# Performance work log

Measured on AMD Instinct MI355X. Metric: run time of the kernel, lower is better.

Reference implementation:

```python
import jax, jax.numpy as jnp
import numpy as np

K = 9            # base neighbors
MAX_DILATION = 3


def setup_inputs() -> dict:
    key = jax.random.key(0)
    x = jax.random.normal(key, (64, 256, 1024), dtype=jnp.float32)  # (B, C, N)
    return {"x": x, "layer_idx": 8}


def reference(x, layer_idx):
    # x: (B, C, N); layer_idx: python int
    B, C, N = x.shape
    dilation = min(layer_idx // 4 + 1, MAX_DILATION)
    k_d = K * dilation

    pts = jnp.transpose(x, (0, 2, 1))  # (B, N, C) points per graph segment
    # squared euclidean pairwise distances (same neighbor ordering as euclidean)
    sq = jnp.sum(pts * pts, axis=-1)                       # (B, N)
    d2 = sq[:, :, None] + sq[:, None, :] \
         - 2.0 * jnp.einsum('bnc,bmc->bnm', pts, pts)      # (B, N, N)

    # k_d nearest neighbors of each node (self included, as in DGL bruteforce knn)
    _, idx = jax.lax.top_k(-d2, k_d)                       # (B, N, k_d)

    # segmented graph: offset node ids per batch element
    offs = (jnp.arange(B) * N)[:, None, None]
    src = (idx + offs).reshape(-1)                         # neighbor -> node edges
    dst = jnp.repeat(jnp.arange(B * N), k_d)

    # dilation: take every `dilation`-th edge; since k_d = K*dilation and each
    # node's edges are contiguous, every node keeps exactly K edges
    src_d = src[::dilation]
    dst_d = dst[::dilation]
    # eval mode: no stochastic edge dropout; include_self=False -> no added self loops
    return src_d, dst_d
```

## Files before the change

kernel.cpp:

```cpp
#include <hip/hip_runtime.h>


typedef __bf16 bf16x8 __attribute__((ext_vector_type(8)));
typedef float  f32x4  __attribute__((ext_vector_type(4)));
typedef unsigned int u32;

#define B_   64
#define C_   256
#define N_   1024
#define NSRC (B_ * N_ * 9)

#define STRIDE_I 1088
#define REGION_W 8704

__device__ __forceinline__ u32 umin_(u32 a, u32 b) { return a < b ? a : b; }
__device__ __forceinline__ u32 umax_(u32 a, u32 b) { return a > b ? a : b; }

__device__ __forceinline__ void load_lds16(const void* g, void* l) {
    __builtin_amdgcn_global_load_lds((const __attribute__((address_space(1))) void*)g,
                                     (__attribute__((address_space(3))) void*)l,
                                     16, 0, 0);
}

__global__ __launch_bounds__(256, 4) void trans_kernel(const float* __restrict__ X,
                                                       unsigned short* __restrict__ XT,
                                                       float* __restrict__ NRM) {
    __shared__ u32 T2[128][66];
    const int tid = threadIdx.x;
    const int b   = blockIdx.x >> 4;
    const int n0  = (blockIdx.x & 15) * 64;

    {
        const int cpl = tid >> 4;
        const int s   = tid & 15;
#pragma unroll
        for (int it = 0; it < 8; ++it) {
            const int c0 = it * 32 + cpl * 2;
            const float* src = X + ((size_t)b * C_ + c0) * N_ + n0 + s * 4;
            float4 f0 = *(const float4*)(src);
            float4 f1 = *(const float4*)(src + N_);
            const float a0[4] = {f0.x, f0.y, f0.z, f0.w};
            const float a1[4] = {f1.x, f1.y, f1.z, f1.w};
            u32 pk[4];
#pragma unroll
            for (int j = 0; j < 4; ++j) {
                u32 u0 = __float_as_uint(a0[j]);
                u32 u1 = __float_as_uint(a1[j]);
                u32 b0 = (u0 + 0x7FFFu + ((u0 >> 16) & 1u)) >> 16;
                u32 b1 = (u1 + 0x7FFFu + ((u1 >> 16) & 1u)) >> 16;
                pk[j] = b0 | (b1 << 16);
            }
            *(uint4*)&T2[it * 16 + cpl][s * 4] = make_uint4(pk[0], pk[1], pk[2], pk[3]);
        }
    }
    __syncthreads();

    {
        const int rr = tid >> 2, p = tid & 3;
        unsigned short* xtrow = XT + ((size_t)b * N_ + n0 + rr) * C_;
        float nsq = 0.f;
#pragma unroll
        for (int j = 0; j < 8; ++j) {
            u32 x0 = T2[j * 16 + 4 * p + 0][rr];
            u32 x1 = T2[j * 16 + 4 * p + 1][rr];
            u32 x2 = T2[j * 16 + 4 * p + 2][rr];
            u32 x3 = T2[j * 16 + 4 * p + 3][rr];
            const u32 xs[4] = {x0, x1, x2, x3};
#pragma unroll
            for (int q = 0; q < 4; ++q) {
                float lo = __uint_as_float(xs[q] << 16);
                float hi = __uint_as_float(xs[q] & 0xFFFF0000u);
                nsq = fmaf(lo, lo, fmaf(hi, hi, nsq));
            }
            *(uint4*)((char*)xtrow + j * 64 + p * 16) = make_uint4(x0, x1, x2, x3);
        }
        nsq += __shfl_xor(nsq, 1);
        nsq += __shfl_xor(nsq, 2);
        if (p == 0) NRM[b * N_ + n0 + rr] = nsq;
    }
}

#define SORT8(v)                                                              \
    do {                                                                      \
        u32 mn, mx;                                                           \
        mn = umin_(v[0], v[4]); mx = umax_(v[0], v[4]); v[0] = mn; v[4] = mx; \
        mn = umin_(v[1], v[5]); mx = umax_(v[1], v[5]); v[1] = mn; v[5] = mx; \
        mn = umin_(v[2], v[6]); mx = umax_(v[2], v[6]); v[2] = mn; v[6] = mx; \
        mn = umin_(v[3], v[7]); mx = umax_(v[3], v[7]); v[3] = mn; v[7] = mx; \
        mn = umin_(v[0], v[2]); mx = umax_(v[0], v[2]); v[0] = mn; v[2] = mx; \
        mn = umin_(v[1], v[3]); mx = umax_(v[1], v[3]); v[1] = mn; v[3] = mx; \
        mn = umin_(v[4], v[6]); mx = umax_(v[4], v[6]); v[4] = mn; v[6] = mx; \
        mn = umin_(v[5], v[7]); mx = umax_(v[5], v[7]); v[5] = mn; v[7] = mx; \
        mn = umin_(v[0], v[1]); mx = umax_(v[0], v[1]); v[0] = mn; v[1] = mx; \
        mn = umin_(v[2], v[3]); mx = umax_(v[2], v[3]); v[2] = mn; v[3] = mx; \
        mn = umin_(v[4], v[5]); mx = umax_(v[4], v[5]); v[4] = mn; v[5] = mx; \
        mn = umin_(v[6], v[7]); mx = umax_(v[6], v[7]); v[6] = mn; v[7] = mx; \
    } while (0)

__global__ __launch_bounds__(256, 4) void knn_mfma_kernel(const unsigned short* __restrict__ XT,
                                                          const float* __restrict__ NRM,
                                                          int* __restrict__ out) {
    __shared__ __align__(1024) char Bt[4 * REGION_W];

    const int tid  = threadIdx.x;
    const int lane = tid & 63;
    const int w    = tid >> 6;

    const int bi = blockIdx.x;
    const int b  = (bi & 7) + 8 * (bi >> 7);
    const int n0 = ((bi >> 3) & 15) * 64;

    const int lrow = lane & 15;
    const int g    = lane >> 4;
    const bool odd = lane & 1;
    const bool hiP = (lane >> 1) & 1;

    const unsigned short* xtb = XT + (size_t)b * N_ * C_;
    const float* nrmb = NRM + b * N_;

    bf16x8 afr[8];
    {
        const unsigned short* ap = xtb + (n0 + w * 16 + lrow) * C_ + g * 8;
#pragma unroll
        for (int kc = 0; kc < 8; ++kc)
            afr[kc] = *(const bf16x8*)(ap + kc * 32);
    }

    u32 L[4][6];
#pragma unroll
    for (int r = 0; r < 4; ++r)
#pragma unroll
        for (int i = 0; i < 6; ++i) L[r][i] = 0xFFFFFFFFu;

    char* const ldsw = Bt + w * REGION_W;
    const int lh   = lane >> 5;
    const int col0 = (lane & 31) * 16;

#pragma unroll 1
    for (int c = 0; c < 16; ++c) {
        {
            const char* gb = (const char*)(xtb + (size_t)(c * 64 + w * 16) * C_);
#pragma unroll
            for (int i = 0; i < 8; ++i) {
                const int rt  = i * 2 + lh;
                const int col = (col0 - rt * 16) & 511;
                load_lds16(gb + (size_t)rt * 512 + col, ldsw + i * STRIDE_I);
            }
        }
        __syncthreads();

#pragma unroll
        for (int t = 0; t < 4; ++t) {
            const char* rbase = Bt + t * REGION_W + (lrow >> 1) * STRIDE_I + (lrow & 1) * 512;
            f32x4 acc = {0.f, 0.f, 0.f, 0.f};
#pragma unroll
            for (int kc = 0; kc < 8; ++kc) {
                bf16x8 bfr = *(const bf16x8*)(rbase + ((kc * 64 + g * 16 + lrow * 16) & 511));
                acc = __builtin_amdgcn_mfma_f32_16x16x32_bf16(afr[kc], bfr, acc, 0, 0, 0);
            }
            const int m = c * 64 + t * 16 + lrow;
            const float nm = nrmb[m];
#pragma unroll
            for (int r = 0; r < 4; ++r) {
                float f = fmaf(-2.f, acc[r], nm);
                u32 u = __float_as_uint(f);
                u = u ^ ((u32)((int)u >> 31) | 0x80000000u);
                u32 cur = (u & 0xFFFFFC00u) | (u32)m;
#pragma unroll
                for (int i = 0; i < 6; ++i) {
                    u32 lo = umin_(L[r][i], cur);
                    u32 hi = umax_(L[r][i], cur);
                    L[r][i] = lo; cur = hi;
                }
            }
        }
        __syncthreads();
    }

    int* out_src = out;
    int* out_dst = out + NSRC;
#pragma unroll
    for (int r = 0; r < 4; ++r) {
        u32 v[8], t1[8];
#pragma unroll
        for (int i = 0; i < 6; ++i) v[i] = L[r][i];
        v[6] = 0xFFFFFFFFu; v[7] = 0xFFFFFFFFu;

#pragma unroll
        for (int i = 0; i < 8; ++i) t1[i] = __shfl_xor(v[i], 1);
#pragma unroll
        for (int i = 0; i < 8; ++i) {
            u32 mn = umin_(v[i], t1[7 - i]);
            u32 mx = umax_(v[i], t1[7 - i]);
            v[i] = odd ? mx : mn;
        }
        SORT8(v);

#pragma unroll
        for (int i = 0; i < 8; ++i) t1[i] = __shfl_xor(v[i], 3);
#pragma unroll
        for (int i = 0; i < 8; ++i) {
            u32 mn = umin_(v[i], t1[7 - i]);
            u32 mx = umax_(v[i], t1[7 - i]);
            v[i] = hiP ? mx : mn;
        }
#pragma unroll
        for (int i = 0; i < 8; ++i) t1[i] = __shfl_xor(v[i], 1);
#pragma unroll
        for (int i = 0; i < 8; ++i)
            v[i] = odd ? umax_(v[i], t1[i]) : umin_(v[i], t1[i]);
        SORT8(v);

#pragma unroll
        for (int s = 0; s < 2; ++s) {
            const int mask = s ? 11 : 7;
#pragma unroll
            for (int i = 0; i < 8; ++i) t1[i] = __shfl_xor(v[i], mask);
#pragma unroll
            for (int i = 0; i < 8; ++i) v[i] = umin_(v[i], t1[7 - i]);
#pragma unroll
            for (int i = 0; i < 8; ++i) t1[i] = __shfl_xor(v[i], 2);
#pragma unroll
            for (int i = 0; i < 8; ++i)
                v[i] = hiP ? umax_(v[i], t1[i]) : umin_(v[i], t1[i]);
#pragma unroll
            for (int i = 0; i < 8; ++i) t1[i] = __shfl_xor(v[i], 1);
#pragma unroll
            for (int i = 0; i < 8; ++i)
                v[i] = odd ? umax_(v[i], t1[i]) : umin_(v[i], t1[i]);
            SORT8(v);
        }

        if ((lane & 12) == 0) {
            const int rank0 = (hiP ? 16 : 0) + (odd ? 8 : 0);
            const int obase = (b * N_ + n0 + w * 16 + 4 * g + r) * 9;
#pragma unroll
            for (int i = 0; i < 8; ++i) {
                const int rank = rank0 + i;
                if (rank < 25 && (rank % 3) == 0)
                    out_src[obase + rank / 3] = (b << 10) | (int)(v[i] & 1023u);
            }
        }
    }

    const int jbase = (b * N_ + n0) * 9;
    for (int idx = tid; idx < 576; idx += 256)
        out_dst[jbase + idx] = (jbase + idx) / 9;
}

__global__ __launch_bounds__(256, 2) void knn_kernel(const float* __restrict__ X,
                                                     int* __restrict__ out) {
    __shared__ float smem[16 * N_];
    const int tid = threadIdx.x;
    const int b  = blockIdx.x >> 6;
    const int n0 = (blockIdx.x & 63) * 16;
    const float* __restrict__ xb = X + (size_t)b * C_ * N_;
#pragma unroll
    for (int i = 0; i < 16; ++i) {
        int f = tid + i * 256;
        int c = f >> 4, qq = f & 15;
        smem[f] = xb[c * N_ + n0 + qq];
    }
    __syncthreads();
    float acc[16][4];
#pragma unroll
    for (int q = 0; q < 16; ++q) { acc[q][0] = acc[q][1] = acc[q][2] = acc[q][3] = 0.f; }
    float nrm[4] = {0.f, 0.f, 0.f, 0.f};
    for (int c = 0; c < C_; ++c) {
        const float* __restrict__ xc = xb + c * N_;
        float bv0 = xc[tid], bv1 = xc[tid + 256], bv2 = xc[tid + 512], bv3 = xc[tid + 768];
        const float4* A4 = reinterpret_cast<const float4*>(smem + c * 16);
        float4 a0 = A4[0], a1 = A4[1], a2 = A4[2], a3 = A4[3];
        float aq[16] = {a0.x, a0.y, a0.z, a0.w, a1.x, a1.y, a1.z, a1.w,
                        a2.x, a2.y, a2.z, a2.w, a3.x, a3.y, a3.z, a3.w};
#pragma unroll
        for (int q = 0; q < 16; ++q) {
            acc[q][0] = fmaf(aq[q], bv0, acc[q][0]);
            acc[q][1] = fmaf(aq[q], bv1, acc[q][1]);
            acc[q][2] = fmaf(aq[q], bv2, acc[q][2]);
            acc[q][3] = fmaf(aq[q], bv3, acc[q][3]);
        }
        nrm[0] = fmaf(bv0, bv0, nrm[0]); nrm[1] = fmaf(bv1, bv1, nrm[1]);
        nrm[2] = fmaf(bv2, bv2, nrm[2]); nrm[3] = fmaf(bv3, bv3, nrm[3]);
    }
    __syncthreads();
#pragma unroll
    for (int q = 0; q < 16; ++q) {
        smem[q * N_ + tid]       = nrm[0] - 2.f * acc[q][0];
        smem[q * N_ + tid + 256] = nrm[1] - 2.f * acc[q][1];
        smem[q * N_ + tid + 512] = nrm[2] - 2.f * acc[q][2];
        smem[q * N_ + tid + 768] = nrm[3] - 2.f * acc[q][3];
    }
    __syncthreads();
    const int lane = tid & 63;
    const int w    = tid >> 6;
    int* out_src = out;
    int* out_dst = out + NSRC;
    for (int q = w; q < 16; q += 4) {
        float v[16];
#pragma unroll
        for (int i = 0; i < 16; ++i) v[i] = smem[q * N_ + lane + i * 64];
        float lv = v[0]; int ls = 0;
#pragma unroll
        for (int i = 1; i < 16; ++i) { if (v[i] < lv) { lv = v[i]; ls = i; } }
        int lm = lane + (ls << 6);
        const int obase = (b * N_ + n0 + q) * 9;
#pragma unroll
        for (int r = 0; r < 25; ++r) {
            float bv = lv; int bm = lm;
#pragma unroll
            for (int off = 32; off >= 1; off >>= 1) {
                float ov = __shfl_xor(bv, off);
                int   om = __shfl_xor(bm, off);
                if (ov < bv || (ov == bv && om < bm)) { bv = ov; bm = om; }
            }
            if ((r % 3) == 0 && lane == 0) out_src[obase + r / 3] = b * N_ + bm;
            if (bm == lm) {
#pragma unroll
                for (int i = 0; i < 16; ++i) { if (i == ls) v[i] = 3.4e38f; }
                lv = v[0]; ls = 0;
#pragma unroll
                for (int i = 1; i < 16; ++i) { if (v[i] < lv) { lv = v[i]; ls = i; } }
                lm = lane + (ls << 6);
            }
        }
    }
    const int jbase = (b * N_ + n0) * 9;
    if (tid < 16 * 9) out_dst[jbase + tid] = (jbase + tid) / 9;
}

extern "C" void kernel_launch(void* const* d_in, const int* in_sizes, int n_in,
                              void* d_out, int out_size, void* d_ws, size_t ws_size,
                              hipStream_t stream) {
    (void)in_sizes; (void)n_in; (void)out_size;
    const float* X = (const float*)d_in[0];
    int* out = (int*)d_out;
    const size_t xt_bytes  = (size_t)B_ * N_ * C_ * 2;
    const size_t nrm_bytes = (size_t)B_ * N_ * 4;
    if (ws_size >= xt_bytes + nrm_bytes) {
        unsigned short* XT = (unsigned short*)d_ws;
        float* NRM = (float*)((char*)d_ws + xt_bytes);
        trans_kernel<<<dim3(B_ * 16), dim3(256), 0, stream>>>(X, XT, NRM);
        knn_mfma_kernel<<<dim3(B_ * 16), dim3(256), 0, stream>>>(XT, NRM, out);
    } else {
        knn_kernel<<<dim3(B_ * 64), dim3(256), 0, stream>>>(X, out);
    }
}
```

Measured before the change: 169.7 us.

## Double-buffer LDS tiles, bias norms positive, and parallelize top-6 insertion

Restructures the candidate loop into 32 chunks of 32 columns with double-buffered LDS, prefetching the next chunk while the current one is processed, which removes one barrier per iteration and overlaps loads with MFMA work. Adds 512 to each squared norm so distances stay positive, which lets the code drop the sign-flip transform on the float key. The top-6 insertion is rewritten as independent min/max pairs instead of a serial chain, shortening the dependency depth. The positivity offset assumes distances never drop below -512, and the added bias lowers float precision for the fixed-point key.

```diff
diff --git a/kernel.cpp b/kernel.cpp
--- a/kernel.cpp
+++ b/kernel.cpp
@@ -11,7 +11,7 @@
 #define NSRC (B_ * N_ * 9)
 
 #define STRIDE_I 1088
-#define REGION_W 8704
+#define BUFB     17408
 
 __device__ __forceinline__ u32 umin_(u32 a, u32 b) { return a < b ? a : b; }
 __device__ __forceinline__ u32 umax_(u32 a, u32 b) { return a > b ? a : b; }
@@ -76,7 +76,7 @@
         }
         nsq += __shfl_xor(nsq, 1);
         nsq += __shfl_xor(nsq, 2);
-        if (p == 0) NRM[b * N_ + n0 + rr] = nsq;
+        if (p == 0) NRM[b * N_ + n0 + rr] = nsq + 512.0f;
     }
 }
 
@@ -100,7 +100,7 @@
 __global__ __launch_bounds__(256, 4) void knn_mfma_kernel(const unsigned short* __restrict__ XT,
                                                           const float* __restrict__ NRM,
                                                           int* __restrict__ out) {
-    __shared__ __align__(1024) char Bt[4 * REGION_W];
+    __shared__ __align__(1024) char Bt[2 * BUFB];
 
     const int tid  = threadIdx.x;
     const int lane = tid & 63;
@@ -132,46 +132,63 @@
 #pragma unroll
         for (int i = 0; i < 6; ++i) L[r][i] = 0xFFFFFFFFu;
 
-    char* const ldsw = Bt + w * REGION_W;
     const int lh   = lane >> 5;
     const int col0 = (lane & 31) * 16;
 
+    {
+        const char* gb = (const char*)(xtb + (size_t)(w * 8) * C_);
+        char* ldsw = Bt + (w * 4) * STRIDE_I;
+#pragma unroll
+        for (int i = 0; i < 4; ++i) {
+            const int rt  = i * 2 + lh;
+            const int col = (col0 - (((w * 8 + rt) & 15) * 16)) & 511;
+            load_lds16(gb + (size_t)rt * 512 + col, ldsw + i * STRIDE_I);
+        }
+    }
+    __syncthreads();
+
 #pragma unroll 1
-    for (int c = 0; c < 16; ++c) {
-        {
-            const char* gb = (const char*)(xtb + (size_t)(c * 64 + w * 16) * C_);
-#pragma unroll
-            for (int i = 0; i < 8; ++i) {
+    for (int c = 0; c < 32; ++c) {
+        const float nm0 = nrmb[c * 32 + lrow];
+        const float nm1 = nrmb[c * 32 + 16 + lrow];
+
+        if (c < 31) {
+            const int cn = c + 1;
+            const char* gb = (const char*)(xtb + (size_t)(cn * 32 + w * 8) * C_);
+            char* ldsw = Bt + (cn & 1) * BUFB + (w * 4) * STRIDE_I;
+#pragma unroll
+            for (int i = 0; i < 4; ++i) {
                 const int rt  = i * 2 + lh;
-                const int col = (col0 - rt * 16) & 511;
+                const int col = (col0 - (((w * 8 + rt) & 15) * 16)) & 511;
                 load_lds16(gb + (size_t)rt * 512 + col, ldsw + i * STRIDE_I);
             }
         }
-        __syncthreads();
-
-#pragma unroll
-        for (int t = 0; t < 4; ++t) {
-            const char* rbase = Bt + t * REGION_W + (lrow >> 1) * STRIDE_I + (lrow & 1) * 512;
+
+        const char* bufc = Bt + (c & 1) * BUFB;
+#pragma unroll
+        for (int t = 0; t < 2; ++t) {
+            const char* rbase = bufc + t * 8704 + (lrow >> 1) * STRIDE_I + (lrow & 1) * 512;
             f32x4 acc = {0.f, 0.f, 0.f, 0.f};
 #pragma unroll
             for (int kc = 0; kc < 8; ++kc) {
                 bf16x8 bfr = *(const bf16x8*)(rbase + ((kc * 64 + g * 16 + lrow * 16) & 511));
                 acc = __builtin_amdgcn_mfma_f32_16x16x32_bf16(afr[kc], bfr, acc, 0, 0, 0);
             }
-            const int m = c * 64 + t * 16 + lrow;
-            const float nm = nrmb[m];
+            const int m = c * 32 + t * 16 + lrow;
+            const float nm = t ? nm1 : nm0;
 #pragma unroll
             for (int r = 0; r < 4; ++r) {
                 float f = fmaf(-2.f, acc[r], nm);
                 u32 u = __float_as_uint(f);
-                u = u ^ ((u32)((int)u >> 31) | 0x80000000u);
                 u32 cur = (u & 0xFFFFFC00u) | (u32)m;
-#pragma unroll
-                for (int i = 0; i < 6; ++i) {
-                    u32 lo = umin_(L[r][i], cur);
-                    u32 hi = umax_(L[r][i], cur);
-                    L[r][i] = lo; cur = hi;
-                }
+                u32 p0 = L[r][0], p1 = L[r][1], p2 = L[r][2];
+                u32 p3 = L[r][3], p4 = L[r][4], p5 = L[r][5];
+                L[r][0] = umin_(p0, cur);
+                L[r][1] = umax_(p0, umin_(p1, cur));
+                L[r][2] = umax_(p1, umin_(p2, cur));
+                L[r][3] = umax_(p2, umin_(p3, cur));
+                L[r][4] = umax_(p3, umin_(p4, cur));
+                L[r][5] = umax_(p4, umin_(p5, cur));
             }
         }
         __syncthreads();
```

New measurement: 169.5 us. No clear change (-0.2%).

## Double-buffer LDS key tiles, share B fragments across two query tiles, shrink top-k lists

Applied to the files above, without the earlier changes.

Restructures the KNN MFMA kernel so each wave computes two 16-row query tiles against a shared 16-column key fragment. The 64 key columns per chunk become 32, and their LDS loads are double-buffered so the next chunk streams in during the current MFMA and selection work. Per-lane sorted candidate lists drop from 6 to 5 entries with a branch-free insert. Lists for the two column halves are exchanged and merged between paired waves through LDS. A +512 bias on the norms keeps distances positive, which removes the sign-flip key transform but relies on that bias holding for the input range.

```diff
diff --git a/kernel.cpp b/kernel.cpp
--- a/kernel.cpp
+++ b/kernel.cpp
@@ -11,7 +11,8 @@
 #define NSRC (B_ * N_ * 9)
 
 #define STRIDE_I 1088
-#define REGION_W 8704
+#define BUFB     17408
+#define INF_     0xFFFFFFFFu
 
 __device__ __forceinline__ u32 umin_(u32 a, u32 b) { return a < b ? a : b; }
 __device__ __forceinline__ u32 umax_(u32 a, u32 b) { return a > b ? a : b; }
@@ -25,7 +26,7 @@
 __global__ __launch_bounds__(256, 4) void trans_kernel(const float* __restrict__ X,
                                                        unsigned short* __restrict__ XT,
                                                        float* __restrict__ NRM) {
-    __shared__ u32 T2[128][66];
+    __shared__ u32 T2[128][68];
     const int tid = threadIdx.x;
     const int b   = blockIdx.x >> 4;
     const int n0  = (blockIdx.x & 15) * 64;
@@ -76,7 +77,7 @@
         }
         nsq += __shfl_xor(nsq, 1);
         nsq += __shfl_xor(nsq, 2);
-        if (p == 0) NRM[b * N_ + n0 + rr] = nsq;
+        if (p == 0) NRM[b * N_ + n0 + rr] = nsq + 512.0f;
     }
 }
 
@@ -97,14 +98,26 @@
         mn = umin_(v[6], v[7]); mx = umax_(v[6], v[7]); v[6] = mn; v[7] = mx; \
     } while (0)
 
+#define INS5(Ls, cur_)                                                        \
+    do {                                                                      \
+        u32 p0 = Ls[0], p1 = Ls[1], p2 = Ls[2], p3 = Ls[3], p4 = Ls[4];       \
+        Ls[0] = umin_(p0, cur_);                                              \
+        Ls[1] = umax_(p0, umin_(p1, cur_));                                   \
+        Ls[2] = umax_(p1, umin_(p2, cur_));                                   \
+        Ls[3] = umax_(p2, umin_(p3, cur_));                                   \
+        Ls[4] = umax_(p3, umin_(p4, cur_));                                   \
+    } while (0)
+
 __global__ __launch_bounds__(256, 4) void knn_mfma_kernel(const unsigned short* __restrict__ XT,
                                                           const float* __restrict__ NRM,
                                                           int* __restrict__ out) {
-    __shared__ __align__(1024) char Bt[4 * REGION_W];
+    __shared__ __align__(1024) char Bt[2 * BUFB];
 
     const int tid  = threadIdx.x;
     const int lane = tid & 63;
     const int w    = tid >> 6;
+    const int qpair = w >> 1;
+    const int h     = w & 1;
 
     const int bi = blockIdx.x;
     const int b  = (bi & 7) + 8 * (bi >> 7);
@@ -116,65 +129,112 @@
     const bool hiP = (lane >> 1) & 1;
 
     const unsigned short* xtb = XT + (size_t)b * N_ * C_;
+    const char* xtc = (const char*)xtb;
     const float* nrmb = NRM + b * N_;
 
-    bf16x8 afr[8];
-    {
-        const unsigned short* ap = xtb + (n0 + w * 16 + lrow) * C_ + g * 8;
+    bf16x8 afr[2][8];
+#pragma unroll
+    for (int s = 0; s < 2; ++s) {
+        const unsigned short* ap = xtb + (n0 + qpair * 32 + s * 16 + lrow) * C_ + g * 8;
 #pragma unroll
         for (int kc = 0; kc < 8; ++kc)
-            afr[kc] = *(const bf16x8*)(ap + kc * 32);
-    }
-
-    u32 L[4][6];
-#pragma unroll
-    for (int r = 0; r < 4; ++r)
-#pragma unroll
-        for (int i = 0; i < 6; ++i) L[r][i] = 0xFFFFFFFFu;
-
-    char* const ldsw = Bt + w * REGION_W;
+            afr[s][kc] = *(const bf16x8*)(ap + kc * 32);
+    }
+
+    u32 L[2][4][5];
+#pragma unroll
+    for (int s = 0; s < 2; ++s)
+#pragma unroll
+        for (int r = 0; r < 4; ++r)
+#pragma unroll
+            for (int i = 0; i < 5; ++i) L[s][r][i] = INF_;
+
+    u32 roffv[8];
+#pragma unroll
+    for (int kc = 0; kc < 8; ++kc)
+        roffv[kc] = (u32)(h * 8704 + (lrow >> 1) * STRIDE_I + (lrow & 1) * 512 +
+                          ((kc * 64 + (g + lrow) * 16) & 511));
+
     const int lh   = lane >> 5;
     const int col0 = (lane & 31) * 16;
+    u32 voff[4];
+#pragma unroll
+    for (int i = 0; i < 4; ++i) {
+        const int rt  = i * 2 + lh;
+        const int col = (col0 - (((w * 8 + rt) & 15) * 16)) & 511;
+        voff[i] = (u32)((w * 8 + rt) * 512 + col);
+    }
+    const float* nmp = nrmb + h * 16 + lrow;
+
+#pragma unroll
+    for (int i = 0; i < 4; ++i)
+        load_lds16(xtc + voff[i], Bt + (w * 4 + i) * STRIDE_I);
+#pragma unroll
+    for (int i = 0; i < 4; ++i) voff[i] += 16384;
+    __syncthreads();
+
+#define CHUNK_BODY(c, U)                                                      \
+    {                                                                         \
+        const float nm = nmp[(c) * 32];                                       \
+        if ((c) < 31) {                                                       \
+            _Pragma("unroll")                                                 \
+            for (int i = 0; i < 4; ++i)                                       \
+                load_lds16(xtc + voff[i],                                     \
+                           Bt + ((U) ^ 1) * BUFB + (w * 4 + i) * STRIDE_I);   \
+            _Pragma("unroll")                                                 \
+            for (int i = 0; i < 4; ++i) voff[i] += 16384;                     \
+        }                                                                     \
+        f32x4 acc0 = {0.f, 0.f, 0.f, 0.f};                                    \
+        f32x4 acc1 = {0.f, 0.f, 0.f, 0.f};                                    \
+        _Pragma("unroll")                                                     \
+        for (int kc = 0; kc < 8; ++kc) {                                      \
+            bf16x8 bfr = *(const bf16x8*)(Bt + (U) * BUFB + roffv[kc]);       \
+            acc0 = __builtin_amdgcn_mfma_f32_16x16x32_bf16(afr[0][kc], bfr,   \
+                                                           acc0, 0, 0, 0);    \
+            acc1 = __builtin_amdgcn_mfma_f32_16x16x32_bf16(afr[1][kc], bfr,   \
+                                                           acc1, 0, 0, 0);    \
+        }                                                                     \
+        const u32 m = (u32)((c) * 32 + h * 16 + lrow);                        \
+        _Pragma("unroll")                                                     \
+        for (int r = 0; r < 4; ++r) {                                         \
+            float f = fmaf(-2.f, acc0[r], nm);        \
+            u32 cur = (__float_as_uint(f) & 0xFFFFFC00u) | m;                 \
+            INS5(L[0][r], cur);                                               \
+        }                                                                     \
+        _Pragma("unroll")                                                     \
+        for (int r = 0; r < 4; ++r) {                                         \
+            float f = fmaf(-2.f, acc1[r], nm);                                \
+            u32 cur = (__float_as_uint(f) & 0xFFFFFC00u) | m;                 \
+            INS5(L[1][r], cur);                                               \
+        }                                                                     \
+        __syncthreads();                                                      \
+    }
 
 #pragma unroll 1
-    for (int c = 0; c < 16; ++c) {
-        {
-            const char* gb = (const char*)(xtb + (size_t)(c * 64 + w * 16) * C_);
-#pragma unroll
-            for (int i = 0; i < 8; ++i) {
-                const int rt  = i * 2 + lh;
-                const int col = (col0 - rt * 16) & 511;
-                load_lds16(gb + (size_t)rt * 512 + col, ldsw + i * STRIDE_I);
-            }
-        }
-        __syncthreads();
-
-#pragma unroll
-        for (int t = 0; t < 4; ++t) {
-            const char* rbase = Bt + t * REGION_W + (lrow >> 1) * STRIDE_I + (lrow & 1) * 512;
-            f32x4 acc = {0.f, 0.f, 0.f, 0.f};
-#pragma unroll
-            for (int kc = 0; kc < 8; ++kc) {
-                bf16x8 bfr = *(const bf16x8*)(rbase + ((kc * 64 + g * 16 + lrow * 16) & 511));
-                acc = __builtin_amdgcn_mfma_f32_16x16x32_bf16(afr[kc], bfr, acc, 0, 0, 0);
-            }
-            const int m = c * 64 + t * 16 + lrow;
-            const float nm = nrmb[m];
-#pragma unroll
-            for (int r = 0; r < 4; ++r) {
-                float f = fmaf(-2.f, acc[r], nm);
-                u32 u = __float_as_uint(f);
-                u = u ^ ((u32)((int)u >> 31) | 0x80000000u);
-                u32 cur = (u & 0xFFFFFC00u) | (u32)m;
-#pragma unroll
-                for (int i = 0; i < 6; ++i) {
-                    u32 lo = umin_(L[r][i], cur);
-                    u32 hi = umax_(L[r][i], cur);
-                    L[r][i] = lo; cur = hi;
-                }
-            }
-        }
-        __syncthreads();
+    for (int cp = 0; cp < 16; ++cp) {
+        const int cbase = cp * 2;
+        CHUNK_BODY(cbase, 0);
+        CHUNK_BODY(cbase + 1, 1);
+    }
+#undef CHUNK_BODY
+
+    {
+        const int o = h ^ 1;
+        const u32 mybase = (u32)((w * 64 + lane) * 80);
+#pragma unroll
+        for (int j = 0; j < 5; ++j)
+            *(uint4*)(Bt + mybase + j * 16) =
+                make_uint4(L[o][0][j], L[o][1][j], L[o][2][j], L[o][3][j]);
+    }
+    __syncthreads();
+    u32 P[4][5];
+    {
+        const u32 exbase = (u32)(((w ^ 1) * 64 + lane) * 80);
+#pragma unroll
+        for (int j = 0; j < 5; ++j) {
+            uint4 q = *(const uint4*)(Bt + exbase + j * 16);
+            P[0][j] = q.x; P[1][j] = q.y; P[2][j] = q.z; P[3][j] = q.w;
+        }
     }
 
     int* out_src = out;
@@ -182,9 +242,16 @@
 #pragma unroll
     for (int r = 0; r < 4; ++r) {
         u32 v[8], t1[8];
-#pragma unroll
-        for (int i = 0; i < 6; ++i) v[i] = L[r][i];
-        v[6] = 0xFFFFFFFFu; v[7] = 0xFFFFFFFFu;
+        {
+            u32 a[8], t[8];
+#pragma unroll
+            for (int i = 0; i < 5; ++i) { a[i] = L[h][r][i]; t[i] = P[r][i]; }
+            a[5] = a[6] = a[7] = INF_;
+            t[5] = t[6] = t[7] = INF_;
+#pragma unroll
+            for (int i = 0; i < 8; ++i) v[i] = umin_(a[i], t[7 - i]);
+            SORT8(v);
+        }
 
 #pragma unroll
         for (int i = 0; i < 8; ++i) t1[i] = __shfl_xor(v[i], 1);
@@ -233,7 +300,8 @@
 
         if ((lane & 12) == 0) {
             const int rank0 = (hiP ? 16 : 0) + (odd ? 8 : 0);
-            const int obase = (b * N_ + n0 + w * 16 + 4 * g + r) * 9;
+            const int qrow  = n0 + qpair * 32 + h * 16 + 4 * g + r;
+            const int obase = (b * N_ + qrow) * 9;
 #pragma unroll
             for (int i = 0; i < 8; ++i) {
                 const int rank = rank0 + i;
```

Result: slower. 484.0 us (+185.1%).
